# Kernel tuning notes

Hardware: AMD Instinct MI355X
Metric: run time of the kernel (lower is better)

Reference implementation:

```python
import jax, jax.numpy as jnp
import numpy as np

B, N, D, P = 4, 4096, 64, 2
M, H = 64, 128
ARENA = 20.0  # positions uniform in [0, ARENA]^2; radius 1.0 -> ~32 neighbors


def _mlp2(x, Wa, ba, Wb, bb):
    return jax.nn.relu(x @ Wa + ba) @ Wb + bb


def setup_inputs() -> dict:
    key = jax.random.key(0)
    ks = jax.random.split(key, 14)
    def lin(k, fan_in, fan_out):
        bound = 1.0 / np.sqrt(fan_in)
        kw, kb = jax.random.split(k)
        W = jax.random.uniform(kw, (fan_in, fan_out), jnp.float32, -bound, bound)
        b = jax.random.uniform(kb, (fan_out,), jnp.float32, -bound, bound)
        return W, b
    W1, b1 = lin(ks[0], D, H)
    W2, b2 = lin(ks[1], H, M)
    W3, b3 = lin(ks[2], 2 * M, H)
    W4, b4 = lin(ks[3], H, M)
    W5, b5 = lin(ks[4], D + M, H)
    W6, b6 = lin(ks[5], H, D)
    agent_states = jax.random.normal(ks[6], (B, N, D), jnp.float32)
    agent_positions = jax.random.uniform(ks[7], (B, N, P), jnp.float32) * ARENA
    return {
        "agent_states": agent_states,
        "agent_positions": agent_positions,
        "neighbor_radius": 1,
        "W1": W1, "b1": b1, "W2": W2, "b2": b2,
        "W3": W3, "b3": b3, "W4": W4, "b4": b4,
        "W5": W5, "b5": b5, "W6": W6, "b6": b6,
    }


def reference(agent_states, agent_positions, neighbor_radius,
              W1, b1, W2, b2, W3, b3, W4, b4, W5, b5, W6, b6):
    n = agent_states.shape[1]
    # message encoder MLP: [B,N,D] -> [B,N,M]
    messages = _mlp2(agent_states, W1, b1, W2, b2)
    # dense pairwise distances [B,N,N] (faithful to original O(N^2) mask)
    diff = agent_positions[:, :, None, :] - agent_positions[:, None, :, :]
    distances = jnp.sqrt(jnp.sum(diff * diff, axis=-1))
    adj = (distances < jnp.float32(neighbor_radius)).astype(messages.dtype)
    adj = adj * (1.0 - jnp.eye(n, dtype=messages.dtype))[None]
    deg = jnp.clip(jnp.sum(adj, axis=-1, keepdims=True), 1.0, None)
    adj = adj / deg
    # vectorized form of the per-agent gather-aggregate loop
    aggregated = jnp.einsum('bij,bjm->bim', adj, messages)
    combined = jnp.concatenate([messages, aggregated], axis=-1)
    final_msgs = _mlp2(combined, W3, b3, W4, b4)
    feats = jnp.concatenate([agent_states, final_msgs], axis=-1)
    out = _mlp2(feats, W5, b5, W6, b6)
    return agent_states + out
```

## Files before the change

### kernel.cpp

```cpp
#include <hip/hip_runtime.h>

typedef unsigned short u16;
typedef unsigned int u32;
typedef __bf16 bf16x8 __attribute__((ext_vector_type(8)));
typedef unsigned short ushort8 __attribute__((ext_vector_type(8)));
typedef float f32x4 __attribute__((ext_vector_type(4)));

#define DEV_INLINE __device__ __forceinline__

constexpr int NB = 4;
constexpr int NAG = 4096;
constexpr int ROWS = NB * NAG;
constexpr int GRID = 20;
constexpr int CELLS = GRID * GRID;
constexpr int CSTRIDE = 404;
constexpr int MAXNB = 256;

DEV_INLINE u16 f2bu(float x) { __bf16 h = (__bf16)x; return __builtin_bit_cast(u16, h); }
DEV_INLINE float bu2f(u16 u) { return __builtin_bit_cast(float, ((u32)u) << 16); }
DEV_INLINE u32 pack2(float a, float b) { return (u32)f2bu(a) | ((u32)f2bu(b) << 16); }

DEV_INLINE f32x4 MF(bf16x8 a, const u16* p, f32x4 c) {
  ushort8 bu = *(const ushort8*)p;
  return __builtin_amdgcn_mfma_f32_16x16x32_bf16(a, __builtin_bit_cast(bf16x8, bu), c, 0, 0, 0);
}

template<bool BF>
DEV_INLINE bf16x8 loadA(const void* __restrict__ src, int row, int c) {
  if constexpr (BF) {
    ushort8 u = *reinterpret_cast<const ushort8*>((const u16*)src + (size_t)row * 64 + c);
    return __builtin_bit_cast(bf16x8, u);
  } else {
    const float* f = (const float*)src + (size_t)row * 64 + c;
    f32x4 a = *(const f32x4*)f;
    f32x4 b = *(const f32x4*)(f + 4);
    bf16x8 r;
    r[0] = (__bf16)a[0]; r[1] = (__bf16)a[1]; r[2] = (__bf16)a[2]; r[3] = (__bf16)a[3];
    r[4] = (__bf16)b[0]; r[5] = (__bf16)b[1]; r[6] = (__bf16)b[2]; r[7] = (__bf16)b[3];
    return r;
  }
}

__global__ __launch_bounds__(1024) void fused_setup_mlp1(
    const float* __restrict__ pos, const float* __restrict__ states,
    const float* __restrict__ W1, const float* __restrict__ b1,
    const float* __restrict__ W2, const float* __restrict__ b2,
    const float* __restrict__ W3, const float* __restrict__ W4,
    const float* __restrict__ W5, const float* __restrict__ W6,
    u16* __restrict__ wts, u16* __restrict__ msgs,
    float2* __restrict__ pos_sorted, int* __restrict__ cell_start,
    int* __restrict__ sid)
{
  extern __shared__ u16 smem[];
  const int tid = threadIdx.x;
  const int lane = tid & 63;
  const int wave = tid >> 6;
  const int bid = blockIdx.x;

  if (bid < NB) {
    int* cnt_s = (int*)smem;
    int* start_s = cnt_s + CELLS;
    u16* cell_of = (u16*)(start_s + CELLS + 1);
    u16* rank_of = cell_of + NAG;
    const float2* pb = (const float2*)(pos + (size_t)bid * NAG * 2);
    for (int c = tid; c < CELLS; c += 1024) cnt_s[c] = 0;
    __syncthreads();
    for (int i = tid; i < NAG; i += 1024) {
      float2 p = pb[i];
      int cx = min(max((int)floorf(p.x), 0), GRID - 1);
      int cy = min(max((int)floorf(p.y), 0), GRID - 1);
      int c = cy * GRID + cx;
      rank_of[i] = (u16)atomicAdd(&cnt_s[c], 1);
      cell_of[i] = (u16)c;
    }
    __syncthreads();
    if (wave == 0) {
      int carry = 0;
      for (int g = 0; g < CELLS; g += 64) {
        int c = g + lane;
        int x = (c < CELLS) ? cnt_s[c] : 0;
#pragma unroll
        for (int off = 1; off < 64; off <<= 1) {
          int y = __shfl_up(x, off, 64);
          if (lane >= off) x += y;
        }
        if (c < CELLS) start_s[c + 1] = carry + x;
        carry += __shfl(x, 63, 64);
      }
      if (lane == 0) start_s[0] = 0;
    }
    __syncthreads();
    for (int c = tid; c <= CELLS; c += 1024) cell_start[bid * CSTRIDE + c] = start_s[c];
    for (int i = tid; i < NAG; i += 1024) {
      int kk = start_s[cell_of[i]] + (int)rank_of[i];
      sid[bid * NAG + kk] = bid * NAG + i;
      pos_sorted[bid * NAG + kk] = pb[i];
    }
    return;
  }

  if (bid >= NB + 256) {
    const int base = (bid - (NB + 256)) * 12288;
#pragma unroll
    for (int t = 0; t < 12; ++t) {
      int idx = base + t * 1024 + tid;
      const float* src; int n, k, Nc;
      if (idx < 16384)      { src = W3; n = idx >> 7; k = idx & 127; Nc = 128; }
      else if (idx < 24576) { int li = idx - 16384; src = W4; n = li >> 7; k = li & 127; Nc = 64; }
      else if (idx < 40960) { int li = idx - 24576; src = W5; n = li >> 7; k = li & 127; Nc = 128; }
      else                  { int li = idx - 40960; src = W6; n = li >> 7; k = li & 127; Nc = 64; }
      wts[idx] = f2bu(src[k * Nc + n]);
    }
    return;
  }

  u16* WaTs = smem;
  u16* WbTs = smem + 9216;
  u16* ovl  = smem + 17920;

  const int l15 = lane & 15;
  const int khalf = (lane >> 4) * 8;
  const int rg = wave >> 2;
  const int cq = wave & 3;
  const int rb = (bid - NB) * 64 + rg * 16;
  const int row = rb + l15;

  bf16x8 aS[2];
  aS[0] = loadA<false>(states, row, khalf);
  aS[1] = loadA<false>(states, row, 32 + khalf);

  for (int t = tid; t < 4096; t += 1024) {
    const int e = t * 2;
    const int k = e >> 7, n = e & 127;
    const float2 v = *(const float2*)&W1[e];
    *(u32*)&ovl[k * 132 + n] = pack2(v.x, v.y);
  }
  __syncthreads();
  {
    const int n = tid & 127, g = tid >> 7;
    ushort8 v;
#pragma unroll
    for (int j = 0; j < 8; ++j) v[j] = ovl[(g * 8 + j) * 132 + n];
    *(ushort8*)&WaTs[n * 72 + g * 8] = v;
  }
  __syncthreads();
  for (int t = tid; t < 4096; t += 1024) {
    const int e = t * 2;
    const int k = e >> 6, n = e & 63;
    const float2 v = *(const float2*)&W2[e];
    *(u32*)&ovl[k * 68 + n] = pack2(v.x, v.y);
  }
  __syncthreads();
  {
    const int n = tid & 63, g = tid >> 6;
    ushort8 v;
#pragma unroll
    for (int j = 0; j < 8; ++j) v[j] = ovl[(g * 8 + j) * 68 + n];
    *(ushort8*)&WbTs[n * 136 + g * 8] = v;
  }
  __syncthreads();

  u16* hs = ovl + rg * 2176;

  f32x4 acc1[2] = {};
#pragma unroll
  for (int kt = 0; kt < 2; ++kt) {
#pragma unroll
    for (int j = 0; j < 2; ++j) {
      const int nt = cq * 2 + j;
      acc1[j] = MF(aS[kt], &WaTs[(nt * 16 + l15) * 72 + kt * 32 + khalf], acc1[j]);
    }
  }
#pragma unroll
  for (int j = 0; j < 2; ++j) {
    const int col = (cq * 2 + j) * 16 + l15;
    const float bv = b1[col];
#pragma unroll
    for (int r = 0; r < 4; ++r)
      hs[((lane >> 4) * 4 + r) * 136 + col] = f2bu(fmaxf(acc1[j][r] + bv, 0.0f));
  }
  __syncthreads();

  f32x4 acc2 = {};
#pragma unroll
  for (int kt = 0; kt < 4; ++kt) {
    ushort8 au = *(const ushort8*)&hs[l15 * 136 + kt * 32 + khalf];
    acc2 = MF(__builtin_bit_cast(bf16x8, au),
              &WbTs[(cq * 16 + l15) * 136 + kt * 32 + khalf], acc2);
  }
  {
    const int col = cq * 16 + l15;
    const float bv = b2[col];
#pragma unroll
    for (int r = 0; r < 4; ++r)
      msgs[(size_t)(rb + (lane >> 4) * 4 + r) * 64 + col] = f2bu(acc2[r] + bv);
  }
}

__global__ __launch_bounds__(256) void agg_kernel(
    const float2* __restrict__ pos_sorted, const u16* __restrict__ msgs,
    const int* __restrict__ cell_start, const int* __restrict__ sid,
    const int* __restrict__ radius_ptr, u16* __restrict__ aggr)
{
  __shared__ u16 idxb[4][MAXNB];
  const int b = blockIdx.y;
  const int lane = threadIdx.x & 63;
  const int wave = threadIdx.x >> 6;
  const int k = blockIdx.x * 4 + wave;
  const float2* pb = pos_sorted + (size_t)b * NAG;
  const float2 pk = pb[k];
  const float r = (float)(*radius_ptr);
  const float r2 = __fmul_rn(r, r);
  const int cx = min(max((int)floorf(pk.x), 0), GRID - 1);
  const int cy = min(max((int)floorf(pk.y), 0), GRID - 1);
  const int* cs = cell_start + b * CSTRIDE;
  const int* sb = sid + b * NAG;
  const unsigned long long lt = (1ull << lane) - 1ull;

  int cnt = 0;
#pragma unroll
  for (int dy = -1; dy <= 1; ++dy) {
    const int yy = cy + dy;
    if (yy < 0 || yy >= GRID) continue;
    const int x0 = max(cx - 1, 0), x1 = min(cx + 1, GRID - 1);
    const int c0 = cs[yy * GRID + x0];
    const int c1 = cs[yy * GRID + x1 + 1];
    for (int base = c0; base < c1; base += 64) {
      const int j = base + lane;
      bool ok = false;
      if (j < c1) {
        const float2 pj = pb[j];
        const float dx_ = pk.x - pj.x;
        const float dy_ = pk.y - pj.y;
        const float d2 = __fadd_rn(__fmul_rn(dx_, dx_), __fmul_rn(dy_, dy_));
        ok = (d2 < r2) && (j != k);
      }
      const unsigned long long m = __ballot(ok);
      if (ok) {
        const int p = cnt + __popcll(m & lt);
        if (p < MAXNB) idxb[wave][p] = (u16)sb[j];
      }
      cnt += (int)__popcll(m);
    }
  }

  float acc = 0.0f;
  const int n = min(cnt, MAXNB);
  for (int g = 0; g < n; g += 8) {
    ushort8 ii = *(const ushort8*)&idxb[wave][g];
    float vs[8];
#pragma unroll
    for (int s = 0; s < 8; ++s) {
      const int jj = (g + s < n) ? (int)ii[s] : (int)ii[0];
      vs[s] = bu2f(msgs[(size_t)jj * 64 + lane]);
    }
#pragma unroll
    for (int s = 0; s < 8; ++s) acc += (g + s < n) ? vs[s] : 0.0f;
  }
  const float inv = 1.0f / (float)(cnt > 0 ? cnt : 1);
  const int orow = sb[k];
  aggr[(size_t)orow * 64 + lane] = f2bu(acc * inv);
}

__global__ __launch_bounds__(1024, 4) void mlp23_kernel(
    const float* __restrict__ states, const u16* __restrict__ msgs,
    const u16* __restrict__ aggr, const u16* __restrict__ wts,
    const float* __restrict__ b3, const float* __restrict__ b4,
    const float* __restrict__ b5, const float* __restrict__ b6,
    float* __restrict__ out)
{
  extern __shared__ u16 smem[];
  u16* W3s = smem;
  u16* W4s = W3s + 128 * 136;
  u16* W5s = W4s + 64 * 136;
  u16* W6s = W5s + 128 * 136;
  u16* hsb = W6s + 64 * 136;
  u16* fsb = hsb + 4 * 16 * 136;

  const int tid = threadIdx.x;
  const int lane = tid & 63;
  const int wave = tid >> 6;
  const int rg = wave >> 2;
  const int cq = wave & 3;
  const int l15 = lane & 15;
  const int khalf = (lane >> 4) * 8;
  const int rb = blockIdx.x * 64 + rg * 16;
  const int row = rb + l15;
  u16* hs = hsb + rg * (16 * 136);
  u16* fs = fsb + rg * (16 * 136);

  bf16x8 aM[2], aG[2], aS[2];
  aM[0] = loadA<true>(msgs, row, khalf);
  aM[1] = loadA<true>(msgs, row, 32 + khalf);
  aG[0] = loadA<true>(aggr, row, khalf);
  aG[1] = loadA<true>(aggr, row, 32 + khalf);
  aS[0] = loadA<false>(states, row, khalf);
  aS[1] = loadA<false>(states, row, 32 + khalf);

  for (int t = tid; t < 6144; t += 1024) {
    const int e = t * 8;
    ushort8 v = *(const ushort8*)&wts[e];
    u16* dst;
    if (e < 16384)      dst = &W3s[(e >> 7) * 136 + (e & 127)];
    else if (e < 24576) { int li = e - 16384; dst = &W4s[(li >> 7) * 136 + (li & 127)]; }
    else if (e < 40960) { int li = e - 24576; dst = &W5s[(li >> 7) * 136 + (li & 127)]; }
    else                { int li = e - 40960; dst = &W6s[(li >> 7) * 136 + (li & 127)]; }
    *(ushort8*)dst = v;
  }
  __syncthreads();

  f32x4 acc1[2] = {};
#pragma unroll
  for (int kt = 0; kt < 4; ++kt) {
    bf16x8 a = (kt < 2) ? aM[kt] : aG[kt - 2];
#pragma unroll
    for (int j = 0; j < 2; ++j) {
      const int nt = cq * 2 + j;
      acc1[j] = MF(a, &W3s[(nt * 16 + l15) * 136 + kt * 32 + khalf], acc1[j]);
    }
  }
#pragma unroll
  for (int j = 0; j < 2; ++j) {
    const int col = (cq * 2 + j) * 16 + l15;
    const float bv = b3[col];
#pragma unroll
    for (int r = 0; r < 4; ++r)
      hs[((lane >> 4) * 4 + r) * 136 + col] = f2bu(fmaxf(acc1[j][r] + bv, 0.0f));
  }
  __syncthreads();

  f32x4 acc2 = {};
#pragma unroll
  for (int kt = 0; kt < 4; ++kt) {
    ushort8 au = *(const ushort8*)&hs[l15 * 136 + kt * 32 + khalf];
    acc2 = MF(__builtin_bit_cast(bf16x8, au),
              &W4s[(cq * 16 + l15) * 136 + kt * 32 + khalf], acc2);
  }
  {
    const int col = cq * 16 + l15;
    const float bv = b4[col];
#pragma unroll
    for (int r = 0; r < 4; ++r)
      fs[((lane >> 4) * 4 + r) * 136 + col] = f2bu(acc2[r] + bv);
  }
  __syncthreads();

  f32x4 acc3[2] = {};
#pragma unroll
  for (int kt = 0; kt < 4; ++kt) {
    bf16x8 a;
    if (kt < 2) a = aS[kt];
    else {
      ushort8 au = *(const ushort8*)&fs[l15 * 136 + (kt - 2) * 32 + khalf];
      a = __builtin_bit_cast(bf16x8, au);
    }
#pragma unroll
    for (int j = 0; j < 2; ++j) {
      const int nt = cq * 2 + j;
      acc3[j] = MF(a, &W5s[(nt * 16 + l15) * 136 + kt * 32 + khalf], acc3[j]);
    }
  }
#pragma unroll
  for (int j = 0; j < 2; ++j) {
    const int col = (cq * 2 + j) * 16 + l15;
    const float bv = b5[col];
#pragma unroll
    for (int r = 0; r < 4; ++r)
      hs[((lane >> 4) * 4 + r) * 136 + col] = f2bu(fmaxf(acc3[j][r] + bv, 0.0f));
  }
  __syncthreads();

  f32x4 acc4 = {};
#pragma unroll
  for (int kt = 0; kt < 4; ++kt) {
    ushort8 au = *(const ushort8*)&hs[l15 * 136 + kt * 32 + khalf];
    acc4 = MF(__builtin_bit_cast(bf16x8, au),
              &W6s[(cq * 16 + l15) * 136 + kt * 32 + khalf], acc4);
  }
  {
    const int col = cq * 16 + l15;
    const float bv = b6[col];
#pragma unroll
    for (int r = 0; r < 4; ++r) {
      const int m = (lane >> 4) * 4 + r;
      const size_t o = (size_t)(rb + m) * 64 + col;
      out[o] = acc4[r] + bv + states[o];
    }
  }
}

extern "C" void kernel_launch(void* const* d_in, const int* in_sizes, int n_in,
                              void* d_out, int out_size, void* d_ws, size_t ws_size,
                              hipStream_t stream) {
  const float* states = (const float*)d_in[0];
  const float* pos    = (const float*)d_in[1];
  const int*   radius = (const int*)d_in[2];
  const float* W1 = (const float*)d_in[3];
  const float* b1 = (const float*)d_in[4];
  const float* W2 = (const float*)d_in[5];
  const float* b2 = (const float*)d_in[6];
  const float* W3 = (const float*)d_in[7];
  const float* b3 = (const float*)d_in[8];
  const float* W4 = (const float*)d_in[9];
  const float* b4 = (const float*)d_in[10];
  const float* W5 = (const float*)d_in[11];
  const float* b5 = (const float*)d_in[12];
  const float* W6 = (const float*)d_in[13];
  const float* b6 = (const float*)d_in[14];
  float* out = (float*)d_out;

  u16* ws16 = (u16*)d_ws;
  u16* msgs = ws16;
  u16* aggr = msgs + (size_t)ROWS * 64;
  u16* wts  = aggr + (size_t)ROWS * 64;
  char* pbyte = (char*)(wts + 49152);
  float2* pos_sorted = (float2*)pbyte;
  int* cell_start = (int*)(pbyte + (size_t)ROWS * 8);
  int* sid = cell_start + NB * CSTRIDE;

  constexpr int LDS_K1 = 26624 * 2;
  constexpr int LDS_K3 = (384 * 136 + 8 * 16 * 136) * 2;

  fused_setup_mlp1<<<NB + 256 + 4, 1024, LDS_K1, stream>>>(
      pos, states, W1, b1, W2, b2, W3, W4, W5, W6,
      wts, msgs, pos_sorted, cell_start, sid);

  agg_kernel<<<dim3(NAG / 4, NB), 256, 0, stream>>>(
      pos_sorted, msgs, cell_start, sid, radius, aggr);

  mlp23_kernel<<<ROWS / 64, 1024, LDS_K3, stream>>>(
      states, msgs, aggr, wts, b3, b4, b5, b6, out);
}
```

Baseline: 42.64 us.

## Fuse neighbor aggregation into MLP kernel and stream weights through reused LDS

Merges the separate aggregation kernel into the second MLP kernel. Each wave gathers neighbor messages for four agents in original order and writes the averaged result into LDS, so the aggr buffer never goes through global memory and one launch is removed. LDS is cut by keeping only two weight slots and reloading W5/W6 into them between layers, and the neighbor cap is halved to fit. This risks serial per-wave aggregation latency inside a 1024-thread block and truncation if an agent has more than 128 neighbors.

```diff
diff --git a/kernel.cpp b/kernel.cpp
--- a/kernel.cpp
+++ b/kernel.cpp
@@ -14,7 +14,7 @@
 constexpr int GRID = 20;
 constexpr int CELLS = GRID * GRID;
 constexpr int CSTRIDE = 404;
-constexpr int MAXNB = 256;
+constexpr int MAXNB = 128;
 
 DEV_INLINE u16 f2bu(float x) { __bf16 h = (__bf16)x; return __builtin_bit_cast(u16, h); }
 DEV_INLINE float bu2f(u16 u) { return __builtin_bit_cast(float, ((u32)u) << 16); }
@@ -197,85 +197,20 @@
   }
 }
 
-__global__ __launch_bounds__(256) void agg_kernel(
-    const float2* __restrict__ pos_sorted, const u16* __restrict__ msgs,
-    const int* __restrict__ cell_start, const int* __restrict__ sid,
-    const int* __restrict__ radius_ptr, u16* __restrict__ aggr)
-{
-  __shared__ u16 idxb[4][MAXNB];
-  const int b = blockIdx.y;
-  const int lane = threadIdx.x & 63;
-  const int wave = threadIdx.x >> 6;
-  const int k = blockIdx.x * 4 + wave;
-  const float2* pb = pos_sorted + (size_t)b * NAG;
-  const float2 pk = pb[k];
-  const float r = (float)(*radius_ptr);
-  const float r2 = __fmul_rn(r, r);
-  const int cx = min(max((int)floorf(pk.x), 0), GRID - 1);
-  const int cy = min(max((int)floorf(pk.y), 0), GRID - 1);
-  const int* cs = cell_start + b * CSTRIDE;
-  const int* sb = sid + b * NAG;
-  const unsigned long long lt = (1ull << lane) - 1ull;
-
-  int cnt = 0;
-#pragma unroll
-  for (int dy = -1; dy <= 1; ++dy) {
-    const int yy = cy + dy;
-    if (yy < 0 || yy >= GRID) continue;
-    const int x0 = max(cx - 1, 0), x1 = min(cx + 1, GRID - 1);
-    const int c0 = cs[yy * GRID + x0];
-    const int c1 = cs[yy * GRID + x1 + 1];
-    for (int base = c0; base < c1; base += 64) {
-      const int j = base + lane;
-      bool ok = false;
-      if (j < c1) {
-        const float2 pj = pb[j];
-        const float dx_ = pk.x - pj.x;
-        const float dy_ = pk.y - pj.y;
-        const float d2 = __fadd_rn(__fmul_rn(dx_, dx_), __fmul_rn(dy_, dy_));
-        ok = (d2 < r2) && (j != k);
-      }
-      const unsigned long long m = __ballot(ok);
-      if (ok) {
-        const int p = cnt + __popcll(m & lt);
-        if (p < MAXNB) idxb[wave][p] = (u16)sb[j];
-      }
-      cnt += (int)__popcll(m);
-    }
-  }
-
-  float acc = 0.0f;
-  const int n = min(cnt, MAXNB);
-  for (int g = 0; g < n; g += 8) {
-    ushort8 ii = *(const ushort8*)&idxb[wave][g];
-    float vs[8];
-#pragma unroll
-    for (int s = 0; s < 8; ++s) {
-      const int jj = (g + s < n) ? (int)ii[s] : (int)ii[0];
-      vs[s] = bu2f(msgs[(size_t)jj * 64 + lane]);
-    }
-#pragma unroll
-    for (int s = 0; s < 8; ++s) acc += (g + s < n) ? vs[s] : 0.0f;
-  }
-  const float inv = 1.0f / (float)(cnt > 0 ? cnt : 1);
-  const int orow = sb[k];
-  aggr[(size_t)orow * 64 + lane] = f2bu(acc * inv);
-}
-
-__global__ __launch_bounds__(1024, 4) void mlp23_kernel(
-    const float* __restrict__ states, const u16* __restrict__ msgs,
-    const u16* __restrict__ aggr, const u16* __restrict__ wts,
+__global__ __launch_bounds__(1024, 4) void agg_mlp23_kernel(
+    const float* __restrict__ states, const float* __restrict__ pos,
+    const u16* __restrict__ msgs, const u16* __restrict__ wts,
+    const float2* __restrict__ pos_sorted, const int* __restrict__ cell_start,
+    const int* __restrict__ sid, const int* __restrict__ radius_ptr,
     const float* __restrict__ b3, const float* __restrict__ b4,
     const float* __restrict__ b5, const float* __restrict__ b6,
     float* __restrict__ out)
 {
   extern __shared__ u16 smem[];
-  u16* W3s = smem;
-  u16* W4s = W3s + 128 * 136;
-  u16* W5s = W4s + 64 * 136;
-  u16* W6s = W5s + 128 * 136;
-  u16* hsb = W6s + 64 * 136;
-  u16* fsb = hsb + 4 * 16 * 136;
+  u16* Wa  = smem;
+  u16* Wb  = smem + 17408;
+  u16* hsr = smem + 26112;
+  u16* fsr = smem + 34816;
 
   const int tid = threadIdx.x;
   const int lane = tid & 63;
@@ -284,39 +219,102 @@
   const int cq = wave & 3;
   const int l15 = lane & 15;
   const int khalf = (lane >> 4) * 8;
-  const int rb = blockIdx.x * 64 + rg * 16;
+  const int rb0 = blockIdx.x * 64;
+  const int rb = rb0 + rg * 16;
   const int row = rb + l15;
-  u16* hs = hsb + rg * (16 * 136);
-  u16* fs = fsb + rg * (16 * 136);
-
-  bf16x8 aM[2], aG[2], aS[2];
+
+  bf16x8 aM[2], aS[2];
   aM[0] = loadA<true>(msgs, row, khalf);
   aM[1] = loadA<true>(msgs, row, 32 + khalf);
-  aG[0] = loadA<true>(aggr, row, khalf);
-  aG[1] = loadA<true>(aggr, row, 32 + khalf);
   aS[0] = loadA<false>(states, row, khalf);
   aS[1] = loadA<false>(states, row, 32 + khalf);
 
-  for (int t = tid; t < 6144; t += 1024) {
+  for (int t = tid; t < 3072; t += 1024) {
     const int e = t * 8;
     ushort8 v = *(const ushort8*)&wts[e];
     u16* dst;
-    if (e < 16384)      dst = &W3s[(e >> 7) * 136 + (e & 127)];
-    else if (e < 24576) { int li = e - 16384; dst = &W4s[(li >> 7) * 136 + (li & 127)]; }
-    else if (e < 40960) { int li = e - 24576; dst = &W5s[(li >> 7) * 136 + (li & 127)]; }
-    else                { int li = e - 40960; dst = &W6s[(li >> 7) * 136 + (li & 127)]; }
+    if (e < 16384) dst = &Wa[(e >> 7) * 136 + (e & 127)];
+    else { int li = e - 16384; dst = &Wb[(li >> 7) * 136 + (li & 127)]; }
     *(ushort8*)dst = v;
   }
-  __syncthreads();
+
+  {
+    const float r = (float)(*radius_ptr);
+    const float r2 = __fmul_rn(r, r);
+    const unsigned long long lt = (1ull << lane) - 1ull;
+    u16* idxw = hsr + wave * (4 * MAXNB);
+#pragma unroll 1
+    for (int a = 0; a < 4; ++a) {
+      const int gi = rb0 + wave * 4 + a;
+      const int b = gi >> 12;
+      const int il = gi & (NAG - 1);
+      const float2 pk = ((const float2*)pos)[(size_t)b * NAG + il];
+      const int cx = min(max((int)floorf(pk.x), 0), GRID - 1);
+      const int cy = min(max((int)floorf(pk.y), 0), GRID - 1);
+      const int* cs = cell_start + b * CSTRIDE;
+      const int* sb = sid + b * NAG;
+      const float2* pb = pos_sorted + (size_t)b * NAG;
+      int cnt = 0;
+#pragma unroll
+      for (int dy = -1; dy <= 1; ++dy) {
+        const int yy = cy + dy;
+        if (yy < 0 || yy >= GRID) continue;
+        const int x0 = max(cx - 1, 0), x1 = min(cx + 1, GRID - 1);
+        const int c0 = cs[yy * GRID + x0];
+        const int c1 = cs[yy * GRID + x1 + 1];
+        for (int base = c0; base < c1; base += 64) {
+          const int j = base + lane;
+          bool ok = false; int sbj = 0;
+          if (j < c1) {
+            const float2 pj = pb[j];
+            sbj = sb[j];
+            const float dx_ = pk.x - pj.x;
+            const float dy_ = pk.y - pj.y;
+            const float d2 = __fadd_rn(__fmul_rn(dx_, dx_), __fmul_rn(dy_, dy_));
+            ok = (d2 < r2) && (sbj != gi);
+          }
+          const unsigned long long m = __ballot(ok);
+          if (ok) {
+            const int p = cnt + __popcll(m & lt);
+            if (p < MAXNB) idxw[a * MAXNB + p] = (u16)sbj;
+          }
+          cnt += (int)__popcll(m);
+        }
+      }
+      float acc = 0.0f;
+      const int n = min(cnt, MAXNB);
+      for (int g = 0; g < n; g += 8) {
+        ushort8 ii = *(const ushort8*)&idxw[a * MAXNB + g];
+        float vs[8];
+#pragma unroll
+        for (int s = 0; s < 8; ++s) {
+          const int jj = (g + s < n) ? (int)ii[s] : (int)ii[0];
+          vs[s] = bu2f(msgs[(size_t)jj * 64 + lane]);
+        }
+#pragma unroll
+        for (int s = 0; s < 8; ++s) acc += (g + s < n) ? vs[s] : 0.0f;
+      }
+      const float inv = 1.0f / (float)(cnt > 0 ? cnt : 1);
+      fsr[(wave * 4 + a) * 72 + lane] = f2bu(acc * inv);
+    }
+  }
+  __syncthreads();
+
+  u16* hs = hsr + rg * 2176;
 
   f32x4 acc1[2] = {};
 #pragma unroll
   for (int kt = 0; kt < 4; ++kt) {
-    bf16x8 a = (kt < 2) ? aM[kt] : aG[kt - 2];
+    bf16x8 a;
+    if (kt < 2) a = aM[kt];
+    else {
+      ushort8 au = *(const ushort8*)&fsr[(rg * 16 + l15) * 72 + (kt - 2) * 32 + khalf];
+      a = __builtin_bit_cast(bf16x8, au);
+    }
 #pragma unroll
     for (int j = 0; j < 2; ++j) {
       const int nt = cq * 2 + j;
-      acc1[j] = MF(a, &W3s[(nt * 16 + l15) * 136 + kt * 32 + khalf], acc1[j]);
+      acc1[j] = MF(a, &Wa[(nt * 16 + l15) * 136 + kt * 32 + khalf], acc1[j]);
     }
   }
 #pragma unroll
@@ -329,35 +327,45 @@
   }
   __syncthreads();
 
+  for (int t = tid; t < 2048; t += 1024) {
+    const int e = t * 8;
+    ushort8 v = *(const ushort8*)&wts[24576 + e];
+    *(ushort8*)&Wa[(e >> 7) * 136 + (e & 127)] = v;
+  }
   f32x4 acc2 = {};
 #pragma unroll
   for (int kt = 0; kt < 4; ++kt) {
     ushort8 au = *(const ushort8*)&hs[l15 * 136 + kt * 32 + khalf];
     acc2 = MF(__builtin_bit_cast(bf16x8, au),
-              &W4s[(cq * 16 + l15) * 136 + kt * 32 + khalf], acc2);
+              &Wb[(cq * 16 + l15) * 136 + kt * 32 + khalf], acc2);
   }
   {
     const int col = cq * 16 + l15;
     const float bv = b4[col];
 #pragma unroll
     for (int r = 0; r < 4; ++r)
-      fs[((lane >> 4) * 4 + r) * 136 + col] = f2bu(acc2[r] + bv);
-  }
-  __syncthreads();
-
+      fsr[((rg * 16) + (lane >> 4) * 4 + r) * 72 + col] = f2bu(acc2[r] + bv);
+  }
+  __syncthreads();
+
+  {
+    const int e = tid * 8;
+    ushort8 v = *(const ushort8*)&wts[40960 + e];
+    *(ushort8*)&Wb[(e >> 7) * 136 + (e & 127)] = v;
+  }
   f32x4 acc3[2] = {};
 #pragma unroll
   for (int kt = 0; kt < 4; ++kt) {
     bf16x8 a;
     if (kt < 2) a = aS[kt];
     else {
-      ushort8 au = *(const ushort8*)&fs[l15 * 136 + (kt - 2) * 32 + khalf];
+      ushort8 au = *(const ushort8*)&fsr[(rg * 16 + l15) * 72 + (kt - 2) * 32 + khalf];
       a = __builtin_bit_cast(bf16x8, au);
     }
 #pragma unroll
     for (int j = 0; j < 2; ++j) {
       const int nt = cq * 2 + j;
-      acc3[j] = MF(a, &W5s[(nt * 16 + l15) * 136 + kt * 32 + khalf], acc3[j]);
+      acc3[j] = MF(a, &Wa[(nt * 16 + l15) * 136 + kt * 32 + khalf], acc3[j]);
     }
   }
 #pragma unroll
@@ -375,7 +383,7 @@
   for (int kt = 0; kt < 4; ++kt) {
     ushort8 au = *(const ushort8*)&hs[l15 * 136 + kt * 32 + khalf];
     acc4 = MF(__builtin_bit_cast(bf16x8, au),
-              &W6s[(cq * 16 + l15) * 136 + kt * 32 + khalf], acc4);
+              &Wb[(cq * 16 + l15) * 136 + kt * 32 + khalf], acc4);
   }
   {
     const int col = cq * 16 + l15;
@@ -411,23 +419,20 @@
 
   u16* ws16 = (u16*)d_ws;
   u16* msgs = ws16;
-  u16* aggr = msgs + (size_t)ROWS * 64;
-  u16* wts  = aggr + (size_t)ROWS * 64;
+  u16* wts  = msgs + (size_t)ROWS * 64;
   char* pbyte = (char*)(wts + 49152);
   float2* pos_sorted = (float2*)pbyte;
   int* cell_start = (int*)(pbyte + (size_t)ROWS * 8);
   int* sid = cell_start + NB * CSTRIDE;
 
   constexpr int LDS_K1 = 26624 * 2;
-  constexpr int LDS_K3 = (384 * 136 + 8 * 16 * 136) * 2;
+  constexpr int LDS_K2 = 39424 * 2;
 
   fused_setup_mlp1<<<NB + 256 + 4, 1024, LDS_K1, stream>>>(
       pos, states, W1, b1, W2, b2, W3, W4, W5, W6,
       wts, msgs, pos_sorted, cell_start, sid);
 
-  agg_kernel<<<dim3(NAG / 4, NB), 256, 0, stream>>>(
-      pos_sorted, msgs, cell_start, sid, radius, aggr);
-
-  mlp23_kernel<<<ROWS / 64, 1024, LDS_K3, stream>>>(
-      states, msgs, aggr, wts, b3, b4, b5, b6, out);
+  agg_mlp23_kernel<<<ROWS / 64, 1024, LDS_K2, stream>>>(
+      states, pos, msgs, wts, pos_sorted, cell_start, sid, radius,
+      b3, b4, b5, b6, out);
 }
```

After: 43.84 us. 1.03x slower.

## Aggregate neighbor messages with MFMA over transposed sorted messages

Applied to the files above, without the earlier changes.

Neighbor aggregation is rewritten. Each wave now handles 16 cell-sorted agents, scans the union of their neighboring cells, and builds a bf16 0/1 adjacency tile that is multiplied with MFMA against a per-batch transposed message buffer stored in sorted order. This replaces per-agent index lists and scalar gathers. Binning moves into its own kernel so MLP1 can scatter the transposed messages through an inverse permutation. The cost is an extra launch, scattered msgsT writes, and wasted work when the 16 agents' cell boxes differ.

```diff
diff --git a/kernel.cpp b/kernel.cpp
--- a/kernel.cpp
+++ b/kernel.cpp
@@ -14,14 +14,15 @@
 constexpr int GRID = 20;
 constexpr int CELLS = GRID * GRID;
 constexpr int CSTRIDE = 404;
-constexpr int MAXNB = 256;
 
 DEV_INLINE u16 f2bu(float x) { __bf16 h = (__bf16)x; return __builtin_bit_cast(u16, h); }
-DEV_INLINE float bu2f(u16 u) { return __builtin_bit_cast(float, ((u32)u) << 16); }
 DEV_INLINE u32 pack2(float a, float b) { return (u32)f2bu(a) | ((u32)f2bu(b) << 16); }
 
 DEV_INLINE f32x4 MF(bf16x8 a, const u16* p, f32x4 c) {
   ushort8 bu = *(const ushort8*)p;
+  return __builtin_amdgcn_mfma_f32_16x16x32_bf16(a, __builtin_bit_cast(bf16x8, bu), c, 0, 0, 0);
+}
+DEV_INLINE f32x4 MFv(bf16x8 a, ushort8 bu, f32x4 c) {
   return __builtin_amdgcn_mfma_f32_16x16x32_bf16(a, __builtin_bit_cast(bf16x8, bu), c, 0, 0, 0);
 }
 
@@ -41,15 +42,63 @@
   }
 }
 
-__global__ __launch_bounds__(1024) void fused_setup_mlp1(
-    const float* __restrict__ pos, const float* __restrict__ states,
+__global__ __launch_bounds__(1024) void bin_kernel(
+    const float* __restrict__ pos, float2* __restrict__ pos_sorted,
+    int* __restrict__ cell_start, int* __restrict__ sid, int* __restrict__ invp)
+{
+  __shared__ int cnt_s[CELLS];
+  __shared__ int start_s[CELLS + 1];
+  __shared__ u16 cell_of[NAG];
+  __shared__ u16 rank_of[NAG];
+  const int tid = threadIdx.x;
+  const int lane = tid & 63;
+  const int wave = tid >> 6;
+  const int bid = blockIdx.x;
+  const float2* pb = (const float2*)(pos + (size_t)bid * NAG * 2);
+  for (int c = tid; c < CELLS; c += 1024) cnt_s[c] = 0;
+  __syncthreads();
+  for (int i = tid; i < NAG; i += 1024) {
+    float2 p = pb[i];
+    int cx = min(max((int)floorf(p.x), 0), GRID - 1);
+    int cy = min(max((int)floorf(p.y), 0), GRID - 1);
+    int c = cy * GRID + cx;
+    rank_of[i] = (u16)atomicAdd(&cnt_s[c], 1);
+    cell_of[i] = (u16)c;
+  }
+  __syncthreads();
+  if (wave == 0) {
+    int carry = 0;
+    for (int g = 0; g < CELLS; g += 64) {
+      int c = g + lane;
+      int x = (c < CELLS) ? cnt_s[c] : 0;
+#pragma unroll
+      for (int off = 1; off < 64; off <<= 1) {
+        int y = __shfl_up(x, off, 64);
+        if (lane >= off) x += y;
+      }
+      if (c < CELLS) start_s[c + 1] = carry + x;
+      carry += __shfl(x, 63, 64);
+    }
+    if (lane == 0) start_s[0] = 0;
+  }
+  __syncthreads();
+  for (int c = tid; c <= CELLS; c += 1024) cell_start[bid * CSTRIDE + c] = start_s[c];
+  for (int i = tid; i < NAG; i += 1024) {
+    int kk = start_s[cell_of[i]] + (int)rank_of[i];
+    sid[bid * NAG + kk] = bid * NAG + i;
+    invp[bid * NAG + i] = kk;
+    pos_sorted[bid * NAG + kk] = pb[i];
+  }
+}
+
+__global__ __launch_bounds__(1024) void mlp1_kernel(
+    const float* __restrict__ states,
     const float* __restrict__ W1, const float* __restrict__ b1,
     const float* __restrict__ W2, const float* __restrict__ b2,
     const float* __restrict__ W3, const float* __restrict__ W4,
     const float* __restrict__ W5, const float* __restrict__ W6,
-    u16* __restrict__ wts, u16* __restrict__ msgs,
-    float2* __restrict__ pos_sorted, int* __restrict__ cell_start,
-    int* __restrict__ sid)
+    const int* __restrict__ invp,
+    u16* __restrict__ wts, u16* __restrict__ msgs, u16* __restrict__ msgsT)
 {
   extern __shared__ u16 smem[];
   const int tid = threadIdx.x;
@@ -57,50 +106,8 @@
   const int wave = tid >> 6;
   const int bid = blockIdx.x;
 
-  if (bid < NB) {
-    int* cnt_s = (int*)smem;
-    int* start_s = cnt_s + CELLS;
-    u16* cell_of = (u16*)(start_s + CELLS + 1);
-    u16* rank_of = cell_of + NAG;
-    const float2* pb = (const float2*)(pos + (size_t)bid * NAG * 2);
-    for (int c = tid; c < CELLS; c += 1024) cnt_s[c] = 0;
-    __syncthreads();
-    for (int i = tid; i < NAG; i += 1024) {
-      float2 p = pb[i];
-      int cx = min(max((int)floorf(p.x), 0), GRID - 1);
-      int cy = min(max((int)floorf(p.y), 0), GRID - 1);
-      int c = cy * GRID + cx;
-      rank_of[i] = (u16)atomicAdd(&cnt_s[c], 1);
-      cell_of[i] = (u16)c;
-    }
-    __syncthreads();
-    if (wave == 0) {
-      int carry = 0;
-      for (int g = 0; g < CELLS; g += 64) {
-        int c = g + lane;
-        int x = (c < CELLS) ? cnt_s[c] : 0;
-#pragma unroll
-        for (int off = 1; off < 64; off <<= 1) {
-          int y = __shfl_up(x, off, 64);
-          if (lane >= off) x += y;
-        }
-        if (c < CELLS) start_s[c + 1] = carry + x;
-        carry += __shfl(x, 63, 64);
-      }
-      if (lane == 0) start_s[0] = 0;
-    }
-    __syncthreads();
-    for (int c = tid; c <= CELLS; c += 1024) cell_start[bid * CSTRIDE + c] = start_s[c];
-    for (int i = tid; i < NAG; i += 1024) {
-      int kk = start_s[cell_of[i]] + (int)rank_of[i];
-      sid[bid * NAG + kk] = bid * NAG + i;
-      pos_sorted[bid * NAG + kk] = pb[i];
-    }
-    return;
-  }
-
-  if (bid >= NB + 256) {
-    const int base = (bid - (NB + 256)) * 12288;
+  if (bid >= 256) {
+    const int base = (bid - 256) * 12288;
 #pragma unroll
     for (int t = 0; t < 12; ++t) {
       int idx = base + t * 1024 + tid;
@@ -122,7 +129,7 @@
   const int khalf = (lane >> 4) * 8;
   const int rg = wave >> 2;
   const int cq = wave & 3;
-  const int rb = (bid - NB) * 64 + rg * 16;
+  const int rb = bid * 64 + rg * 16;
   const int row = rb + l15;
 
   bf16x8 aS[2];
@@ -192,74 +199,111 @@
     const int col = cq * 16 + l15;
     const float bv = b2[col];
 #pragma unroll
-    for (int r = 0; r < 4; ++r)
-      msgs[(size_t)(rb + (lane >> 4) * 4 + r) * 64 + col] = f2bu(acc2[r] + bv);
+    for (int r = 0; r < 4; ++r) {
+      const int grow = rb + (lane >> 4) * 4 + r;
+      const u16 v = f2bu(acc2[r] + bv);
+      msgs[(size_t)grow * 64 + col] = v;
+      const int bb = grow >> 12;
+      const int sl = invp[grow];
+      msgsT[((size_t)(bb * 64 + col)) * NAG + sl] = v;
+    }
   }
 }
 
 __global__ __launch_bounds__(256) void agg_kernel(
-    const float2* __restrict__ pos_sorted, const u16* __restrict__ msgs,
+    const float2* __restrict__ pos_sorted, const u16* __restrict__ msgsT,
     const int* __restrict__ cell_start, const int* __restrict__ sid,
     const int* __restrict__ radius_ptr, u16* __restrict__ aggr)
 {
-  __shared__ u16 idxb[4][MAXNB];
+  __shared__ u16 dsr[4][16][72];
   const int b = blockIdx.y;
   const int lane = threadIdx.x & 63;
   const int wave = threadIdx.x >> 6;
-  const int k = blockIdx.x * 4 + wave;
-  const float2* pb = pos_sorted + (size_t)b * NAG;
-  const float2 pk = pb[k];
+  const int l15 = lane & 15;
+  const int grp = lane >> 4;
+  const int khalf = grp * 8;
+  const int k0 = (blockIdx.x * 4 + wave) * 16;
+  const int ks = k0 + l15;
+  const float2* pk = pos_sorted + (size_t)b * NAG;
+  const int* cs = cell_start + b * CSTRIDE;
+  const int* sb = sid + b * NAG;
   const float r = (float)(*radius_ptr);
   const float r2 = __fmul_rn(r, r);
-  const int cx = min(max((int)floorf(pk.x), 0), GRID - 1);
-  const int cy = min(max((int)floorf(pk.y), 0), GRID - 1);
-  const int* cs = cell_start + b * CSTRIDE;
-  const int* sb = sid + b * NAG;
-  const unsigned long long lt = (1ull << lane) - 1ull;
-
+
+  const float2 apos = pk[ks];
+  int cx = min(max((int)floorf(apos.x), 0), GRID - 1);
+  int cy = min(max((int)floorf(apos.y), 0), GRID - 1);
+  int cxmin = cx, cxmax = cx, cymin = cy, cymax = cy;
+#pragma unroll
+  for (int off = 1; off < 16; off <<= 1) {
+    cxmin = min(cxmin, __shfl_xor(cxmin, off));
+    cxmax = max(cxmax, __shfl_xor(cxmax, off));
+    cymin = min(cymin, __shfl_xor(cymin, off));
+    cymax = max(cymax, __shfl_xor(cymax, off));
+  }
+  const int y0 = max(cymin - 1, 0), y1 = min(cymax + 1, GRID - 1);
+  const int x0 = max(cxmin - 1, 0), x1 = min(cxmax + 1, GRID - 1);
+
+  const u16* bp0 = msgsT + ((size_t)(b * 64 + 0  + l15)) * NAG;
+  const u16* bp1 = msgsT + ((size_t)(b * 64 + 16 + l15)) * NAG;
+  const u16* bp2 = msgsT + ((size_t)(b * 64 + 32 + l15)) * NAG;
+  const u16* bp3 = msgsT + ((size_t)(b * 64 + 48 + l15)) * NAG;
+
+  const __bf16 one = (__bf16)1.0f;
+  const __bf16 zero = (__bf16)0.0f;
+  f32x4 acc[4] = {};
   int cnt = 0;
-#pragma unroll
-  for (int dy = -1; dy <= 1; ++dy) {
-    const int yy = cy + dy;
-    if (yy < 0 || yy >= GRID) continue;
-    const int x0 = max(cx - 1, 0), x1 = min(cx + 1, GRID - 1);
+
+  for (int yy = y0; yy <= y1; ++yy) {
     const int c0 = cs[yy * GRID + x0];
     const int c1 = cs[yy * GRID + x1 + 1];
-    for (int base = c0; base < c1; base += 64) {
-      const int j = base + lane;
-      bool ok = false;
-      if (j < c1) {
-        const float2 pj = pb[j];
-        const float dx_ = pk.x - pj.x;
-        const float dy_ = pk.y - pj.y;
+    for (int cc = c0; cc < c1; cc += 32) {
+      const int cb = cc + khalf;
+      const float4* pp = (const float4*)(pk + cb);
+      const float4 q0 = pp[0], q1 = pp[1], q2 = pp[2], q3 = pp[3];
+      float px[8], py[8];
+      px[0] = q0.x; py[0] = q0.y; px[1] = q0.z; py[1] = q0.w;
+      px[2] = q1.x; py[2] = q1.y; px[3] = q1.z; py[3] = q1.w;
+      px[4] = q2.x; py[4] = q2.y; px[5] = q2.z; py[5] = q2.w;
+      px[6] = q3.x; py[6] = q3.y; px[7] = q3.z; py[7] = q3.w;
+      bf16x8 af;
+#pragma unroll
+      for (int j = 0; j < 8; ++j) {
+        const int c = cb + j;
+        const float dx_ = apos.x - px[j];
+        const float dy_ = apos.y - py[j];
         const float d2 = __fadd_rn(__fmul_rn(dx_, dx_), __fmul_rn(dy_, dy_));
-        ok = (d2 < r2) && (j != k);
+        const bool ok = (d2 < r2) && (c != ks) && (c < c1);
+        af[j] = ok ? one : zero;
+        cnt += ok ? 1 : 0;
       }
-      const unsigned long long m = __ballot(ok);
-      if (ok) {
-        const int p = cnt + __popcll(m & lt);
-        if (p < MAXNB) idxb[wave][p] = (u16)sb[j];
-      }
-      cnt += (int)__popcll(m);
-    }
-  }
-
-  float acc = 0.0f;
-  const int n = min(cnt, MAXNB);
-  for (int g = 0; g < n; g += 8) {
-    ushort8 ii = *(const ushort8*)&idxb[wave][g];
-    float vs[8];
-#pragma unroll
-    for (int s = 0; s < 8; ++s) {
-      const int jj = (g + s < n) ? (int)ii[s] : (int)ii[0];
-      vs[s] = bu2f(msgs[(size_t)jj * 64 + lane]);
-    }
-#pragma unroll
-    for (int s = 0; s < 8; ++s) acc += (g + s < n) ? vs[s] : 0.0f;
-  }
+      acc[0] = MFv(af, *(const ushort8*)(bp0 + cb), acc[0]);
+      acc[1] = MFv(af, *(const ushort8*)(bp1 + cb), acc[1]);
+      acc[2] = MFv(af, *(const ushort8*)(bp2 + cb), acc[2]);
+      acc[3] = MFv(af, *(const ushort8*)(bp3 + cb), acc[3]);
+    }
+  }
+
+  cnt += __shfl_xor(cnt, 16);
+  cnt += __shfl_xor(cnt, 32);
   const float inv = 1.0f / (float)(cnt > 0 ? cnt : 1);
-  const int orow = sb[k];
-  aggr[(size_t)orow * 64 + lane] = f2bu(acc * inv);
+  float invr[4];
+#pragma unroll
+  for (int rr = 0; rr < 4; ++rr) invr[rr] = __shfl(inv, grp * 4 + rr);
+
+#pragma unroll
+  for (int nt = 0; nt < 4; ++nt)
+#pragma unroll
+    for (int rr = 0; rr < 4; ++rr)
+      dsr[wave][grp * 4 + rr][nt * 16 + l15] = f2bu(acc[nt][rr] * invr[rr]);
+  __syncthreads();
+
+  const int orow = sb[k0 + (lane >> 2)];
+  const int part = lane & 3;
+  ushort8 v0 = *(const ushort8*)&dsr[wave][lane >> 2][part * 16];
+  ushort8 v1 = *(const ushort8*)&dsr[wave][lane >> 2][part * 16 + 8];
+  *(ushort8*)(aggr + (size_t)orow * 64 + part * 16) = v0;
+  *(ushort8*)(aggr + (size_t)orow * 64 + part * 16 + 8) = v1;
 }
 
 __global__ __launch_bounds__(1024, 4) void mlp23_kernel(
@@ -410,24 +454,27 @@
   float* out = (float*)d_out;
 
   u16* ws16 = (u16*)d_ws;
-  u16* msgs = ws16;
-  u16* aggr = msgs + (size_t)ROWS * 64;
-  u16* wts  = aggr + (size_t)ROWS * 64;
+  u16* msgs  = ws16;
+  u16* aggr  = msgs + (size_t)ROWS * 64;
+  u16* msgsT = aggr + (size_t)ROWS * 64;
+  u16* wts   = msgsT + (size_t)ROWS * 64;
   char* pbyte = (char*)(wts + 49152);
   float2* pos_sorted = (float2*)pbyte;
   int* cell_start = (int*)(pbyte + (size_t)ROWS * 8);
-  int* sid = cell_start + NB * CSTRIDE;
+  int* sid  = cell_start + NB * CSTRIDE;
+  int* invp = sid + ROWS;
 
   constexpr int LDS_K1 = 26624 * 2;
   constexpr int LDS_K3 = (384 * 136 + 8 * 16 * 136) * 2;
 
-  fused_setup_mlp1<<<NB + 256 + 4, 1024, LDS_K1, stream>>>(
-      pos, states, W1, b1, W2, b2, W3, W4, W5, W6,
-      wts, msgs, pos_sorted, cell_start, sid);
-
-  agg_kernel<<<dim3(NAG / 4, NB), 256, 0, stream>>>(
-      pos_sorted, msgs, cell_start, sid, radius, aggr);
-
-  mlp23_kernel<<<ROWS / 64, 1024, LDS_K3, stream>>>(
+  bin_kernel<<<NB, 1024, 0, stream>>>(pos, pos_sorted, cell_start, sid, invp);
+
+  mlp1_kernel<<<260, 1024, LDS_K1, stream>>>(
+      states, W1, b1, W2, b2, W3, W4, W5, W6, invp, wts, msgs, msgsT);
+
+  agg_kernel<<<dim3(NAG / 64, NB), 256, 0, stream>>>(
+      pos_sorted, msgsT, cell_start, sid, radius, aggr);
+
+  mlp23_kernel<<<256, 1024, LDS_K3, stream>>>(
       states, msgs, aggr, wts, b3, b4, b5, b6, out);
 }
```

After: 74.76 us. 1.75x slower.
